# Kernel optimization log

Measured on AMD Instinct MI355X. Metric: run time of the kernel, lower is better.

The kernel has to match this reference:

```python
import jax, jax.numpy as jnp
import numpy as np

NEG_BIG = -9e15  # matches -9000000000000000.0 in the torch source
ALPHA = 0.2      # LeakyReLU slope


def setup_inputs() -> dict:
    key = jax.random.key(0)
    k1, k2, k3, k4 = jax.random.split(key, 4)
    N, F_in, F_out = 8192, 128, 64
    x = jax.random.normal(k1, (N, F_in), dtype=jnp.float32)
    adj = jax.random.normal(k2, (N, N), dtype=jnp.float32)
    W = jax.random.normal(k3, (F_in, F_out), dtype=jnp.float32) * 0.1
    a = jax.random.normal(k4, (2 * F_out,), dtype=jnp.float32) * 0.1
    return {"x": x, "adj": adj, "W": W, "a": a}


def reference(x, adj, W, a):
    F_out = W.shape[1]
    h = x @ W                      # [N, F_out]
    # a([h_i || h_j]) decomposes into a1.h_i + a2.h_j -> avoid the [N,N,2F] concat
    a1, a2 = a[:F_out], a[F_out:]
    s1 = h @ a1                    # [N] source scores
    s2 = h @ a2                    # [N] target scores
    e = jax.nn.leaky_relu(s1[:, None] + s2[None, :], negative_slope=ALPHA)  # [N, N]
    attention = jnp.where(adj > 0, e, NEG_BIG)
    attention = jax.nn.softmax(attention, axis=1)
    h_prime = attention @ h        # [N, F_out]
    return jax.nn.elu(h_prime)
```

## Files before the change

### kernel.cpp

```cpp
#include <hip/hip_runtime.h>
#include <hip/hip_bf16.h>

#define ALPHA 0.2f
#define NROW 8192

typedef __attribute__((ext_vector_type(4))) float f4;
typedef __attribute__((ext_vector_type(8))) short s8;

__device__ __forceinline__ short f2bf_bits(float x){
    __hip_bfloat16 b = __float2bfloat16(x);
    return __builtin_bit_cast(short, b);
}

__device__ __forceinline__ void gload_lds16(const void* g, void* l){
    __builtin_amdgcn_global_load_lds(
        (const __attribute__((address_space(1))) void*)g,
        (__attribute__((address_space(3))) void*)l, 16, 0, 0);
}

__global__ __launch_bounds__(256) void k_proj(
    const float* __restrict__ x, const float* __restrict__ W, const float* __restrict__ a,
    float* __restrict__ s1,
    float* __restrict__ F1, float* __restrict__ F2, __hip_bfloat16* __restrict__ hpack)
{
    __shared__ float Wsh[128*64];
    __shared__ float xsh[4*128];
    const int t = threadIdx.x;
    const int f = t & 63, ry = t >> 6;
    const int row0 = blockIdx.x * 4;
    for (int i = t; i < 128*64; i += 256) Wsh[i] = W[i];
    for (int i = t; i < 4*128; i += 256) xsh[i] = x[row0*128 + i];
    __syncthreads();
    float acc = 0.f;
    #pragma unroll
    for (int k = 0; k < 128; ++k) acc = fmaf(xsh[ry*128 + k], Wsh[k*64 + f], acc);
    float p1 = acc * a[f], p2 = acc * a[64 + f];
    #pragma unroll
    for (int m = 32; m; m >>= 1){ p1 += __shfl_xor(p1, m, 64); p2 += __shfl_xor(p2, m, 64); }
    const int j = row0 + ry;
    if (f == 0){
        s1[j] = p1;
        F1[j] = __expf(p2); F2[j] = __expf(0.2f * p2);
    }
    const int sc = j >> 5, hg = (j >> 3) & 3, e = j & 7;
    const int fg = f >> 4, lr = f & 15;
    hpack[(((sc*4 + fg)*64) + hg*16 + lr)*8 + e] = __float2bfloat16(acc);
}

__global__ __launch_bounds__(512, 2) void k_gat(
    const float* __restrict__ adj, const float* __restrict__ s1g,
    const float* __restrict__ F1g, const float* __restrict__ F2g,
    const __hip_bfloat16* __restrict__ hpack,
    float* __restrict__ part, float* __restrict__ pden)
{
    __shared__ __attribute__((aligned(16))) char arena[139264];

    const int tid = threadIdx.x;
    const int w = tid >> 6, lane = tid & 63;
    const int lr = lane & 15, hi = lane >> 4;
    const int jslab = blockIdx.x >> 5, igrp = blockIdx.x & 31;

    const s8* hsl = (const s8*)arena;
    float* F1sl = (float*)(arena + 131072);
    float* F2sl = (float*)(arena + 135168);

    const int rbA = igrp*256 + w*16;
    const int rowA = rbA + lr, rowB = rowA + 128;
    const float s1A = s1g[rowA], s1B = s1g[rowB];
    const float E1A = __expf(s1A), E2A = __expf(ALPHA*s1A), T1A = __expf(-s1A);
    const float E1B = __expf(s1B), E2B = __expf(ALPHA*s1B), T1B = __expf(-s1B);

    {
        const s8* hp = (const s8*)hpack + jslab*8192;
        #pragma unroll
        for (int it = 0; it < 16; ++it)
            gload_lds16(hp + w*1024 + it*64 + lane, arena + (w*1024 + it*64)*16);
        #pragma unroll
        for (int k = 0; k < 2; ++k){
            F1sl[tid + k*512] = F1g[jslab*1024 + tid + k*512];
            F2sl[tid + k*512] = F2g[jslab*1024 + tid + k*512];
        }
    }
    __syncthreads();

    const float* padj = adj + (long)(rbA + (lane >> 3))*NROW + jslab*1024 + (lane & 7)*4;
    const unsigned bsh = (unsigned)((lr & 7)*8 + hi*2);
    const int hi8 = hi * 8;

    f4 acc0A={0,0,0,0}, acc1A={0,0,0,0}, acc2A={0,0,0,0}, acc3A={0,0,0,0};
    f4 acc0B={0,0,0,0}, acc1B={0,0,0,0}, acc2B={0,0,0,0}, acc3B={0,0,0,0};
    float lsumA = 0.f, lsumB = 0.f;

    f4 v0S0,v1S0, v0S1,v1S1, v0S2,v1S2, v0S3,v1S3;
    f4 v0S4,v1S4, v0S5,v1S5, v0S6,v1S6, v0S7,v1S7;

#define LOAD(S, st_) do { \
    const long o_ = (long)(((st_) >> 5) * (128*NROW)) + (((st_) & 31) * 32); \
    v0##S = *(const f4*)(padj + o_); \
    v1##S = *(const f4*)(padj + o_ + 8*NROW); \
} while(0)

#define CALCQ(X, cond, g1, g2, qd) { \
    float fz = ((g1) > T1##X) ? (g1) * E1##X : (g2) * E2##X; \
    qd = (cond) ? fz : 0.f; }

#define STEP(X, S, st_) do { \
    unsigned long long c0_ = __ballot(v0##S[0] > 0.f); \
    unsigned long long c1_ = __ballot(v0##S[1] > 0.f); \
    unsigned long long c2_ = __ballot(v0##S[2] > 0.f); \
    unsigned long long c3_ = __ballot(v0##S[3] > 0.f); \
    unsigned long long d0_ = __ballot(v1##S[0] > 0.f); \
    unsigned long long d1_ = __ballot(v1##S[1] > 0.f); \
    unsigned long long d2_ = __ballot(v1##S[2] > 0.f); \
    unsigned long long d3_ = __ballot(v1##S[3] > 0.f); \
    const unsigned u0 = (unsigned)(((lr < 8) ? c0_ : d0_) >> bsh); \
    const unsigned u1 = (unsigned)(((lr < 8) ? c1_ : d1_) >> bsh); \
    const unsigned u2 = (unsigned)(((lr < 8) ? c2_ : d2_) >> bsh); \
    const unsigned u3 = (unsigned)(((lr < 8) ? c3_ : d3_) >> bsh); \
    const int t_ = (st_) & 31; \
    const s8* hb_ = hsl + t_*256; \
    s8 h0 = hb_[lane]; s8 h1 = hb_[64 + lane]; \
    s8 h2 = hb_[128 + lane]; s8 h3 = hb_[192 + lane]; \
    f4 f1a = *(const f4*)&F1sl[t_*32 + hi8]; f4 f1b = *(const f4*)&F1sl[t_*32 + hi8 + 4]; \
    f4 f2a = *(const f4*)&F2sl[t_*32 + hi8]; f4 f2b = *(const f4*)&F2sl[t_*32 + hi8 + 4]; \
    float q0,q1,q2,q3,q4,q5,q6,q7; \
    CALCQ(X, u0 & 1u, f1a[0], f2a[0], q0); CALCQ(X, u1 & 1u, f1a[1], f2a[1], q1); \
    CALCQ(X, u2 & 1u, f1a[2], f2a[2], q2); CALCQ(X, u3 & 1u, f1a[3], f2a[3], q3); \
    CALCQ(X, u0 & 2u, f1b[0], f2b[0], q4); CALCQ(X, u1 & 2u, f1b[1], f2b[1], q5); \
    CALCQ(X, u2 & 2u, f1b[2], f2b[2], q6); CALCQ(X, u3 & 2u, f1b[3], f2b[3], q7); \
    lsum##X += ((q0+q1)+(q2+q3)) + ((q4+q5)+(q6+q7)); \
    s8 af; \
    af[0]=f2bf_bits(q0); af[1]=f2bf_bits(q1); af[2]=f2bf_bits(q2); af[3]=f2bf_bits(q3); \
    af[4]=f2bf_bits(q4); af[5]=f2bf_bits(q5); af[6]=f2bf_bits(q6); af[7]=f2bf_bits(q7); \
    acc0##X = __builtin_amdgcn_mfma_f32_16x16x32_bf16(af, h0, acc0##X, 0, 0, 0); \
    acc1##X = __builtin_amdgcn_mfma_f32_16x16x32_bf16(af, h1, acc1##X, 0, 0, 0); \
    acc2##X = __builtin_amdgcn_mfma_f32_16x16x32_bf16(af, h2, acc2##X, 0, 0, 0); \
    acc3##X = __builtin_amdgcn_mfma_f32_16x16x32_bf16(af, h3, acc3##X, 0, 0, 0); \
} while(0)

#define W14 asm volatile("s_waitcnt vmcnt(14)" ::: "memory")

    LOAD(S0, 0); LOAD(S1, 1); LOAD(S2, 2); LOAD(S3, 3);
    LOAD(S4, 4); LOAD(S5, 5); LOAD(S6, 6); LOAD(S7, 7);

#define ROUND(X, it_) do { \
    const int st = (it_)*8; \
    W14; STEP(X, S0, st    ); LOAD(S0, st + 8); \
    W14; STEP(X, S1, st + 1); LOAD(S1, st + 9); \
    W14; STEP(X, S2, st + 2); LOAD(S2, st + 10); \
    W14; STEP(X, S3, st + 3); LOAD(S3, st + 11); \
    W14; STEP(X, S4, st + 4); LOAD(S4, st + 12); \
    W14; STEP(X, S5, st + 5); LOAD(S5, st + 13); \
    W14; STEP(X, S6, st + 6); LOAD(S6, st + 14); \
    W14; STEP(X, S7, st + 7); LOAD(S7, st + 15); \
} while(0)

    #pragma unroll 1
    for (int it = 0; it < 4; ++it) ROUND(A, it);
    #pragma unroll 1
    for (int it = 4; it < 7; ++it) ROUND(B, it);
    W14;                                          STEP(B, S0, 56);
    asm volatile("s_waitcnt vmcnt(12)" ::: "memory"); STEP(B, S1, 57);
    asm volatile("s_waitcnt vmcnt(10)" ::: "memory"); STEP(B, S2, 58);
    asm volatile("s_waitcnt vmcnt(8)"  ::: "memory"); STEP(B, S3, 59);
    asm volatile("s_waitcnt vmcnt(6)"  ::: "memory"); STEP(B, S4, 60);
    asm volatile("s_waitcnt vmcnt(4)"  ::: "memory"); STEP(B, S5, 61);
    asm volatile("s_waitcnt vmcnt(2)"  ::: "memory"); STEP(B, S6, 62);
    asm volatile("s_waitcnt vmcnt(0)"  ::: "memory"); STEP(B, S7, 63);

#undef LOAD
#undef CALCQ
#undef STEP
#undef W14
#undef ROUND

    lsumA += __shfl_xor(lsumA, 16, 64); lsumA += __shfl_xor(lsumA, 32, 64);
    lsumB += __shfl_xor(lsumB, 16, 64); lsumB += __shfl_xor(lsumB, 32, 64);

    {
        const long pbA = ((long)jslab*NROW + rbA + hi*4)*64 + lr;
        const long pbB = pbA + 128L*64;
        #pragma unroll
        for (int r = 0; r < 4; ++r){
            part[pbA + r*64 +  0] = acc0A[r];
            part[pbA + r*64 + 16] = acc1A[r];
            part[pbA + r*64 + 32] = acc2A[r];
            part[pbA + r*64 + 48] = acc3A[r];
            part[pbB + r*64 +  0] = acc0B[r];
            part[pbB + r*64 + 16] = acc1B[r];
            part[pbB + r*64 + 32] = acc2B[r];
            part[pbB + r*64 + 48] = acc3B[r];
        }
        if (lane < 16){
            pden[jslab*NROW + rbA + lr]       = lsumA;
            pden[jslab*NROW + rbA + 128 + lr] = lsumB;
        }
    }
}

__global__ __launch_bounds__(256) void k_comb(
    const float* __restrict__ part, const float* __restrict__ pden,
    float* __restrict__ out)
{
    const int idx = blockIdx.x*256 + threadIdx.x;
    const int i = idx >> 4, c4 = (idx & 15) << 2;
    f4 sa = {0.f,0.f,0.f,0.f}; float L = 0.f;
    #pragma unroll
    for (int s = 0; s < 8; ++s){
        sa += *(const f4*)&part[((long)s*NROW + i)*64 + c4];
        L  += pden[s*NROW + i];
    }
    const float inv = 1.f / L;
    f4 o;
    #pragma unroll
    for (int e = 0; e < 4; ++e){
        float v = sa[e] * inv;
        o[e] = (v > 0.f) ? v : expm1f(v);
    }
    *(f4*)&out[(long)i*64 + c4] = o;
}

extern "C" void kernel_launch(void* const* d_in, const int* in_sizes, int n_in,
                              void* d_out, int out_size, void* d_ws, size_t ws_size,
                              hipStream_t stream)
{
    const float* x   = (const float*)d_in[0];
    const float* adj = (const float*)d_in[1];
    const float* W   = (const float*)d_in[2];
    const float* a   = (const float*)d_in[3];
    float* out = (float*)d_out;

    char* ws = (char*)d_ws;
    float* s1   = (float*)(ws);
    float* F1   = (float*)(ws + 65536);
    float* F2   = (float*)(ws + 98304);
    __hip_bfloat16* hpack = (__hip_bfloat16*)(ws + 131328);
    float* part = (float*)(ws + 1179904);
    float* pden = (float*)(ws + 17957120);

    k_proj <<<2048,  256, 0, stream>>>(x, W, a, s1, F1, F2, hpack);
    k_gat  <<< 256,  512, 0, stream>>>(adj, s1, F1, F2, hpack, part, pden);
    k_comb <<< 512,  256, 0, stream>>>(part, pden, out);
}
```

Before: 70.68 us.

## Re-tile GAT kernel to wider column slabs with double-buffered h staging

The attention kernel now gives each block 128 rows by a 2048-column slab instead of 256 rows by 1024 columns. The bf16 h tile for the slab is streamed into two LDS buffers and refilled asynchronously between barriers, rather than loaded whole up front. This halves the number of column partials, so the combine kernel reads 4 partial sums instead of 8 and writes less partial traffic. The projection kernel is also changed to process 32 rows per block, which cuts the redundant W loads into LDS. The cost is an extra barrier per sub-slab, and a tighter LDS budget that may limit occupancy.

```diff
diff --git a/kernel.cpp b/kernel.cpp
--- a/kernel.cpp
+++ b/kernel.cpp
@@ -24,27 +24,32 @@
     float* __restrict__ F1, float* __restrict__ F2, __hip_bfloat16* __restrict__ hpack)
 {
     __shared__ float Wsh[128*64];
-    __shared__ float xsh[4*128];
+    __shared__ float xsh[32*128];
     const int t = threadIdx.x;
-    const int f = t & 63, ry = t >> 6;
-    const int row0 = blockIdx.x * 4;
+    const int f = t & 63, wq = t >> 6;
+    const int row0 = blockIdx.x * 32;
     for (int i = t; i < 128*64; i += 256) Wsh[i] = W[i];
-    for (int i = t; i < 4*128; i += 256) xsh[i] = x[row0*128 + i];
+    for (int i = t; i < 32*128; i += 256) xsh[i] = x[row0*128 + i];
     __syncthreads();
-    float acc = 0.f;
-    #pragma unroll
-    for (int k = 0; k < 128; ++k) acc = fmaf(xsh[ry*128 + k], Wsh[k*64 + f], acc);
-    float p1 = acc * a[f], p2 = acc * a[64 + f];
-    #pragma unroll
-    for (int m = 32; m; m >>= 1){ p1 += __shfl_xor(p1, m, 64); p2 += __shfl_xor(p2, m, 64); }
-    const int j = row0 + ry;
-    if (f == 0){
-        s1[j] = p1;
-        F1[j] = __expf(p2); F2[j] = __expf(0.2f * p2);
-    }
-    const int sc = j >> 5, hg = (j >> 3) & 3, e = j & 7;
-    const int fg = f >> 4, lr = f & 15;
-    hpack[(((sc*4 + fg)*64) + hg*16 + lr)*8 + e] = __float2bfloat16(acc);
+    const float a1 = a[f], a2 = a[64 + f];
+    #pragma unroll 1
+    for (int rr = 0; rr < 8; ++rr){
+        const int ry = wq*8 + rr;
+        float acc = 0.f;
+        #pragma unroll
+        for (int k = 0; k < 128; ++k) acc = fmaf(xsh[ry*128 + k], Wsh[k*64 + f], acc);
+        float p1 = acc * a1, p2 = acc * a2;
+        #pragma unroll
+        for (int m = 32; m; m >>= 1){ p1 += __shfl_xor(p1, m, 64); p2 += __shfl_xor(p2, m, 64); }
+        const int j = row0 + ry;
+        if (f == 0){
+            s1[j] = p1;
+            F1[j] = __expf(p2); F2[j] = __expf(0.2f * p2);
+        }
+        const int sc = j >> 5, hg = (j >> 3) & 3, e = j & 7;
+        const int fg = f >> 4, lr = f & 15;
+        hpack[(((sc*4 + fg)*64) + hg*16 + lr)*8 + e] = __float2bfloat16(acc);
+    }
 }
 
 __global__ __launch_bounds__(512, 2) void k_gat(
@@ -53,58 +58,55 @@
     const __hip_bfloat16* __restrict__ hpack,
     float* __restrict__ part, float* __restrict__ pden)
 {
-    __shared__ __attribute__((aligned(16))) char arena[139264];
+    __shared__ __attribute__((aligned(16))) char arena[147456];
 
     const int tid = threadIdx.x;
     const int w = tid >> 6, lane = tid & 63;
     const int lr = lane & 15, hi = lane >> 4;
-    const int jslab = blockIdx.x >> 5, igrp = blockIdx.x & 31;
-
-    const s8* hsl = (const s8*)arena;
+    const int jslab = blockIdx.x >> 6, igrp = blockIdx.x & 63;
+
     float* F1sl = (float*)(arena + 131072);
-    float* F2sl = (float*)(arena + 135168);
-
-    const int rbA = igrp*256 + w*16;
-    const int rowA = rbA + lr, rowB = rowA + 128;
-    const float s1A = s1g[rowA], s1B = s1g[rowB];
-    const float E1A = __expf(s1A), E2A = __expf(ALPHA*s1A), T1A = __expf(-s1A);
-    const float E1B = __expf(s1B), E2B = __expf(ALPHA*s1B), T1B = __expf(-s1B);
-
-    {
-        const s8* hp = (const s8*)hpack + jslab*8192;
-        #pragma unroll
-        for (int it = 0; it < 16; ++it)
-            gload_lds16(hp + w*1024 + it*64 + lane, arena + (w*1024 + it*64)*16);
-        #pragma unroll
-        for (int k = 0; k < 2; ++k){
-            F1sl[tid + k*512] = F1g[jslab*1024 + tid + k*512];
-            F2sl[tid + k*512] = F2g[jslab*1024 + tid + k*512];
-        }
-    }
+    float* F2sl = (float*)(arena + 139264);
+
+    const int rbA = igrp*128 + w*16;
+    const int row = rbA + lr;
+    const float s1r = s1g[row];
+    const float E1 = __expf(s1r), E2 = __expf(ALPHA*s1r), T1 = __expf(-s1r);
+
+#define STAGEH(buf, sw_) do { \
+    const s8* hp_ = (const s8*)hpack + (jslab*64 + (sw_)*16)*256 + w*512 + lane; \
+    char* dst_ = arena + (buf)*65536 + (w*512)*16; \
+    _Pragma("unroll") \
+    for (int it_ = 0; it_ < 8; ++it_) \
+        gload_lds16(hp_ + it_*64, dst_ + it_*1024); \
+} while(0)
+
+    STAGEH(0, 0);
+    *(f4*)&F1sl[tid*4] = *(const f4*)(F1g + jslab*2048 + tid*4);
+    *(f4*)&F2sl[tid*4] = *(const f4*)(F2g + jslab*2048 + tid*4);
     __syncthreads();
 
-    const float* padj = adj + (long)(rbA + (lane >> 3))*NROW + jslab*1024 + (lane & 7)*4;
+    const float* padj = adj + (long)(rbA + (lane >> 3))*NROW + jslab*2048 + (lane & 7)*4;
     const unsigned bsh = (unsigned)((lr & 7)*8 + hi*2);
     const int hi8 = hi * 8;
 
-    f4 acc0A={0,0,0,0}, acc1A={0,0,0,0}, acc2A={0,0,0,0}, acc3A={0,0,0,0};
-    f4 acc0B={0,0,0,0}, acc1B={0,0,0,0}, acc2B={0,0,0,0}, acc3B={0,0,0,0};
-    float lsumA = 0.f, lsumB = 0.f;
+    f4 acc0={0,0,0,0}, acc1={0,0,0,0}, acc2={0,0,0,0}, acc3={0,0,0,0};
+    float lsum = 0.f;
 
     f4 v0S0,v1S0, v0S1,v1S1, v0S2,v1S2, v0S3,v1S3;
     f4 v0S4,v1S4, v0S5,v1S5, v0S6,v1S6, v0S7,v1S7;
 
-#define LOAD(S, st_) do { \
-    const long o_ = (long)(((st_) >> 5) * (128*NROW)) + (((st_) & 31) * 32); \
+#define LOAD(S, s_) do { \
+    const int o_ = (s_) * 32; \
     v0##S = *(const f4*)(padj + o_); \
     v1##S = *(const f4*)(padj + o_ + 8*NROW); \
 } while(0)
 
-#define CALCQ(X, cond, g1, g2, qd) { \
-    float fz = ((g1) > T1##X) ? (g1) * E1##X : (g2) * E2##X; \
+#define CALCQ(cond, g1, g2, qd) { \
+    float fz = ((g1) > T1) ? (g1) * E1 : (g2) * E2; \
     qd = (cond) ? fz : 0.f; }
 
-#define STEP(X, S, st_) do { \
+#define STEP(S, s_) do { \
     unsigned long long c0_ = __ballot(v0##S[0] > 0.f); \
     unsigned long long c1_ = __ballot(v0##S[1] > 0.f); \
     unsigned long long c2_ = __ballot(v0##S[2] > 0.f); \
@@ -117,84 +119,78 @@
     const unsigned u1 = (unsigned)(((lr < 8) ? c1_ : d1_) >> bsh); \
     const unsigned u2 = (unsigned)(((lr < 8) ? c2_ : d2_) >> bsh); \
     const unsigned u3 = (unsigned)(((lr < 8) ? c3_ : d3_) >> bsh); \
-    const int t_ = (st_) & 31; \
-    const s8* hb_ = hsl + t_*256; \
+    const s8* hb_ = (const s8*)(arena + (((s_) >> 4) & 1)*65536) + ((s_) & 15)*256; \
     s8 h0 = hb_[lane]; s8 h1 = hb_[64 + lane]; \
     s8 h2 = hb_[128 + lane]; s8 h3 = hb_[192 + lane]; \
-    f4 f1a = *(const f4*)&F1sl[t_*32 + hi8]; f4 f1b = *(const f4*)&F1sl[t_*32 + hi8 + 4]; \
-    f4 f2a = *(const f4*)&F2sl[t_*32 + hi8]; f4 f2b = *(const f4*)&F2sl[t_*32 + hi8 + 4]; \
+    f4 f1a = *(const f4*)&F1sl[(s_)*32 + hi8]; f4 f1b = *(const f4*)&F1sl[(s_)*32 + hi8 + 4]; \
+    f4 f2a = *(const f4*)&F2sl[(s_)*32 + hi8]; f4 f2b = *(const f4*)&F2sl[(s_)*32 + hi8 + 4]; \
     float q0,q1,q2,q3,q4,q5,q6,q7; \
-    CALCQ(X, u0 & 1u, f1a[0], f2a[0], q0); CALCQ(X, u1 & 1u, f1a[1], f2a[1], q1); \
-    CALCQ(X, u2 & 1u, f1a[2], f2a[2], q2); CALCQ(X, u3 & 1u, f1a[3], f2a[3], q3); \
-    CALCQ(X, u0 & 2u, f1b[0], f2b[0], q4); CALCQ(X, u1 & 2u, f1b[1], f2b[1], q5); \
-    CALCQ(X, u2 & 2u, f1b[2], f2b[2], q6); CALCQ(X, u3 & 2u, f1b[3], f2b[3], q7); \
-    lsum##X += ((q0+q1)+(q2+q3)) + ((q4+q5)+(q6+q7)); \
+    CALCQ(u0 & 1u, f1a[0], f2a[0], q0); CALCQ(u1 & 1u, f1a[1], f2a[1], q1); \
+    CALCQ(u2 & 1u, f1a[2], f2a[2], q2); CALCQ(u3 & 1u, f1a[3], f2a[3], q3); \
+    CALCQ(u0 & 2u, f1b[0], f2b[0], q4); CALCQ(u1 & 2u, f1b[1], f2b[1], q5); \
+    CALCQ(u2 & 2u, f1b[2], f2b[2], q6); CALCQ(u3 & 2u, f1b[3], f2b[3], q7); \
+    lsum += ((q0+q1)+(q2+q3)) + ((q4+q5)+(q6+q7)); \
     s8 af; \
     af[0]=f2bf_bits(q0); af[1]=f2bf_bits(q1); af[2]=f2bf_bits(q2); af[3]=f2bf_bits(q3); \
     af[4]=f2bf_bits(q4); af[5]=f2bf_bits(q5); af[6]=f2bf_bits(q6); af[7]=f2bf_bits(q7); \
-    acc0##X = __builtin_amdgcn_mfma_f32_16x16x32_bf16(af, h0, acc0##X, 0, 0, 0); \
-    acc1##X = __builtin_amdgcn_mfma_f32_16x16x32_bf16(af, h1, acc1##X, 0, 0, 0); \
-    acc2##X = __builtin_amdgcn_mfma_f32_16x16x32_bf16(af, h2, acc2##X, 0, 0, 0); \
-    acc3##X = __builtin_amdgcn_mfma_f32_16x16x32_bf16(af, h3, acc3##X, 0, 0, 0); \
+    acc0 = __builtin_amdgcn_mfma_f32_16x16x32_bf16(af, h0, acc0, 0, 0, 0); \
+    acc1 = __builtin_amdgcn_mfma_f32_16x16x32_bf16(af, h1, acc1, 0, 0, 0); \
+    acc2 = __builtin_amdgcn_mfma_f32_16x16x32_bf16(af, h2, acc2, 0, 0, 0); \
+    acc3 = __builtin_amdgcn_mfma_f32_16x16x32_bf16(af, h3, acc3, 0, 0, 0); \
 } while(0)
 
 #define W14 asm volatile("s_waitcnt vmcnt(14)" ::: "memory")
+#define ROUND8(stb) do { \
+    W14; STEP(S0, (stb)    ); LOAD(S0, (stb) + 8); \
+    W14; STEP(S1, (stb) + 1); LOAD(S1, (stb) + 9); \
+    W14; STEP(S2, (stb) + 2); LOAD(S2, (stb) + 10); \
+    W14; STEP(S3, (stb) + 3); LOAD(S3, (stb) + 11); \
+    W14; STEP(S4, (stb) + 4); LOAD(S4, (stb) + 12); \
+    W14; STEP(S5, (stb) + 5); LOAD(S5, (stb) + 13); \
+    W14; STEP(S6, (stb) + 6); LOAD(S6, (stb) + 14); \
+    W14; STEP(S7, (stb) + 7); LOAD(S7, (stb) + 15); \
+} while(0)
 
     LOAD(S0, 0); LOAD(S1, 1); LOAD(S2, 2); LOAD(S3, 3);
     LOAD(S4, 4); LOAD(S5, 5); LOAD(S6, 6); LOAD(S7, 7);
 
-#define ROUND(X, it_) do { \
-    const int st = (it_)*8; \
-    W14; STEP(X, S0, st    ); LOAD(S0, st + 8); \
-    W14; STEP(X, S1, st + 1); LOAD(S1, st + 9); \
-    W14; STEP(X, S2, st + 2); LOAD(S2, st + 10); \
-    W14; STEP(X, S3, st + 3); LOAD(S3, st + 11); \
-    W14; STEP(X, S4, st + 4); LOAD(S4, st + 12); \
-    W14; STEP(X, S5, st + 5); LOAD(S5, st + 13); \
-    W14; STEP(X, S6, st + 6); LOAD(S6, st + 14); \
-    W14; STEP(X, S7, st + 7); LOAD(S7, st + 15); \
-} while(0)
-
     #pragma unroll 1
-    for (int it = 0; it < 4; ++it) ROUND(A, it);
-    #pragma unroll 1
-    for (int it = 4; it < 7; ++it) ROUND(B, it);
-    W14;                                          STEP(B, S0, 56);
-    asm volatile("s_waitcnt vmcnt(12)" ::: "memory"); STEP(B, S1, 57);
-    asm volatile("s_waitcnt vmcnt(10)" ::: "memory"); STEP(B, S2, 58);
-    asm volatile("s_waitcnt vmcnt(8)"  ::: "memory"); STEP(B, S3, 59);
-    asm volatile("s_waitcnt vmcnt(6)"  ::: "memory"); STEP(B, S4, 60);
-    asm volatile("s_waitcnt vmcnt(4)"  ::: "memory"); STEP(B, S5, 61);
-    asm volatile("s_waitcnt vmcnt(2)"  ::: "memory"); STEP(B, S6, 62);
-    asm volatile("s_waitcnt vmcnt(0)"  ::: "memory"); STEP(B, S7, 63);
+    for (int sw = 0; sw < 3; ++sw){
+        STAGEH((sw + 1) & 1, sw + 1);
+        const int stb = sw * 16;
+        ROUND8(stb); ROUND8(stb + 8);
+        asm volatile("s_barrier" ::: "memory");
+    }
+    ROUND8(48);
+    W14;                                              STEP(S0, 56);
+    asm volatile("s_waitcnt vmcnt(12)" ::: "memory"); STEP(S1, 57);
+    asm volatile("s_waitcnt vmcnt(10)" ::: "memory"); STEP(S2, 58);
+    asm volatile("s_waitcnt vmcnt(8)"  ::: "memory"); STEP(S3, 59);
+    asm volatile("s_waitcnt vmcnt(6)"  ::: "memory"); STEP(S4, 60);
+    asm volatile("s_waitcnt vmcnt(4)"  ::: "memory"); STEP(S5, 61);
+    asm volatile("s_waitcnt vmcnt(2)"  ::: "memory"); STEP(S6, 62);
+    asm volatile("s_waitcnt vmcnt(0)"  ::: "memory"); STEP(S7, 63);
 
 #undef LOAD
 #undef CALCQ
 #undef STEP
 #undef W14
-#undef ROUND
-
-    lsumA += __shfl_xor(lsumA, 16, 64); lsumA += __shfl_xor(lsumA, 32, 64);
-    lsumB += __shfl_xor(lsumB, 16, 64); lsumB += __shfl_xor(lsumB, 32, 64);
+#undef ROUND8
+#undef STAGEH
+
+    lsum += __shfl_xor(lsum, 16, 64);
+    lsum += __shfl_xor(lsum, 32, 64);
 
     {
-        const long pbA = ((long)jslab*NROW + rbA + hi*4)*64 + lr;
-        const long pbB = pbA + 128L*64;
+        const long pb = ((long)jslab*NROW + rbA + hi*4)*64 + lr;
         #pragma unroll
         for (int r = 0; r < 4; ++r){
-            part[pbA + r*64 +  0] = acc0A[r];
-            part[pbA + r*64 + 16] = acc1A[r];
-            part[pbA + r*64 + 32] = acc2A[r];
-            part[pbA + r*64 + 48] = acc3A[r];
-            part[pbB + r*64 +  0] = acc0B[r];
-            part[pbB + r*64 + 16] = acc1B[r];
-            part[pbB + r*64 + 32] = acc2B[r];
-            part[pbB + r*64 + 48] = acc3B[r];
+            part[pb + r*64 +  0] = acc0[r];
+            part[pb + r*64 + 16] = acc1[r];
+            part[pb + r*64 + 32] = acc2[r];
+            part[pb + r*64 + 48] = acc3[r];
         }
-        if (lane < 16){
-            pden[jslab*NROW + rbA + lr]       = lsumA;
-            pden[jslab*NROW + rbA + 128 + lr] = lsumB;
-        }
+        if (lane < 16) pden[jslab*NROW + rbA + lr] = lsum;
     }
 }
 
@@ -206,7 +202,7 @@
     const int i = idx >> 4, c4 = (idx & 15) << 2;
     f4 sa = {0.f,0.f,0.f,0.f}; float L = 0.f;
     #pragma unroll
-    for (int s = 0; s < 8; ++s){
+    for (int s = 0; s < 4; ++s){
         sa += *(const f4*)&part[((long)s*NROW + i)*64 + c4];
         L  += pden[s*NROW + i];
     }
@@ -236,9 +232,9 @@
     float* F2   = (float*)(ws + 98304);
     __hip_bfloat16* hpack = (__hip_bfloat16*)(ws + 131328);
     float* part = (float*)(ws + 1179904);
-    float* pden = (float*)(ws + 17957120);
-
-    k_proj <<<2048,  256, 0, stream>>>(x, W, a, s1, F1, F2, hpack);
-    k_gat  <<< 256,  512, 0, stream>>>(adj, s1, F1, F2, hpack, part, pden);
-    k_comb <<< 512,  256, 0, stream>>>(part, pden, out);
-}
+    float* pden = (float*)(ws + 9568512);
+
+    k_proj <<<256, 256, 0, stream>>>(x, W, a, s1, F1, F2, hpack);
+    k_gat  <<<256, 512, 0, stream>>>(adj, s1, F1, F2, hpack, part, pden);
+    k_comb <<<512, 256, 0, stream>>>(part, pden, out);
+}
```

After: 67.63 us, median of 2. 1.05x faster.
